# Optimization experiments

Hardware: AMD Instinct MI355X
Metric: run time of the kernel (lower is better)

Reference implementation:

```python
import jax, jax.numpy as jnp
import numpy as np

DIM = 192
HEADS = 6
WIN = 7


def conv2d(x, w, b, pad):
    # x: (N,C,H,W), w: (O,I,kh,kw)
    y = jax.lax.conv_general_dilated(
        x, w, window_strides=(1, 1), padding=[(pad, pad), (pad, pad)],
        dimension_numbers=('NCHW', 'OIHW', 'NCHW'))
    return y + b[None, :, None, None]


def setup_inputs() -> dict:
    key = jax.random.key(0)
    ks = jax.random.split(key, 4)
    B, C, H, W = 8, DIM, 128, 128
    D = C // HEADS
    s = lambda fan_in: 1.0 / np.sqrt(fan_in)
    return {
        'x': jax.random.normal(ks[0], (B, C, H, W), jnp.float32),
        'w_qkv': jax.random.normal(ks[1], (3 * C, C, 1, 1), jnp.float32) * s(C),
        'b_qkv': jnp.zeros((3 * C,), jnp.float32),
        'w_attn': jax.random.normal(ks[2], (WIN * WIN, 2 * D, WIN, WIN), jnp.float32) * s(2 * D * WIN * WIN),
        'b_attn': jnp.zeros((WIN * WIN,), jnp.float32),
        'w_proj': jax.random.normal(ks[3], (C, C, 1, 1), jnp.float32) * s(C),
        'b_proj': jnp.zeros((C,), jnp.float32),
    }


def reference(x, w_qkv, b_qkv, w_attn, b_attn, w_proj, b_proj):
    B, C, H, W = x.shape
    D = C // HEADS
    scale = D ** -0.5
    # qkv 1x1 conv -> (B, 3, heads, D, H, W)
    qkv = conv2d(x, w_qkv, b_qkv, 0).reshape(B, 3, HEADS, D, H, W)
    q, v = qkv[:, 0], qkv[:, 2]  # NOTE: original code uses q twice (not k)
    q_flat = q.reshape(B * HEADS, D, H, W)
    qq = jnp.concatenate([q_flat * scale, q_flat], axis=1)  # (B*heads, 2D, H, W)
    # conv-generated local attention logits over winSize^2 positions
    attn = conv2d(qq, w_attn, b_attn, WIN // 2)
    attn = jax.nn.softmax(attn, axis=1).reshape(B, HEADS, WIN * WIN, H, W)
    # sum over window dim of v (broadcast over k) * attn (broadcast over d)
    out = jnp.einsum('bhkxy,bhdxy->bhdxy', attn, v).reshape(B, C, H, W)
    return conv2d(out, w_proj, b_proj, 0)
```

## Files before the change

### kernel.cpp

```cpp
#include <hip/hip_runtime.h>
#include <stdint.h>
#include <stddef.h>


#define CDIM 192
#define HWPX 16384
#define LDS_STRIDE 200

typedef __attribute__((ext_vector_type(8))) short short8;
typedef __attribute__((ext_vector_type(4))) float floatx4;
typedef __attribute__((ext_vector_type(4))) unsigned short ushort4_t;

__device__ __forceinline__ unsigned short f2bf(float f) {
    union { float f; unsigned int u; } v; v.f = f;
    unsigned int r = (v.u + 0x7FFFu + ((v.u >> 16) & 1u)) >> 16;
    return (unsigned short)r;
}

__global__ __launch_bounds__(192) void prep_kernel(
    const float* __restrict__ w_qkv, const float* __restrict__ b_qkv,
    const float* __restrict__ w_proj, const float* __restrict__ b_proj,
    unsigned short* __restrict__ Mb, float* __restrict__ bias)
{
    const int o = blockIdx.x, c = threadIdx.x;
    const float* wpr = w_proj + o * CDIM;
    const float* wv  = w_qkv + 2 * CDIM * CDIM;
    float acc = 0.f;
    #pragma unroll 32
    for (int k = 0; k < CDIM; ++k)
        acc = fmaf(wpr[k], wv[k * CDIM + c], acc);
    Mb[o * CDIM + c] = f2bf(acc);

    __shared__ float red[CDIM];
    red[c] = wpr[c] * b_qkv[2 * CDIM + c];
    __syncthreads();
    if (c < 64) {
        float v = red[c] + red[c + 64] + red[c + 128];
        #pragma unroll
        for (int off = 32; off > 0; off >>= 1) v += __shfl_down(v, off);
        if (c == 0) bias[o] = v + b_proj[o];
    }
}

__global__ __launch_bounds__(256, 2) void fused_kernel(
    const float* __restrict__ x,
    const unsigned short* __restrict__ Mb,
    const float* __restrict__ bias,
    float* __restrict__ out)
{
    __shared__ unsigned short Xl[64 * LDS_STRIDE];

    const int tid = threadIdx.x;
    const int bid = blockIdx.x;
    const int b   = bid >> 8;
    const int p0  = (bid & 255) << 6;

    const int lane = tid & 63;
    const int w    = tid >> 6;
    const int n    = lane & 15;
    const int q    = lane >> 4;

    const float* xb = x + (size_t)b * CDIM * HWPX + p0;
    #pragma unroll
    for (int it = 0; it < 3; ++it) {
        const int slot = it * 256 + tid;
        const int p4   = slot & 15;
        const int cg4  = slot >> 4;
        const float* src = xb + (size_t)(cg4 * 4) * HWPX + p4 * 4;
        floatx4 f0 = *(const floatx4*)(src);
        floatx4 f1 = *(const floatx4*)(src + HWPX);
        floatx4 f2 = *(const floatx4*)(src + 2 * HWPX);
        floatx4 f3 = *(const floatx4*)(src + 3 * HWPX);
        #pragma unroll
        for (int i = 0; i < 4; ++i) {
            ushort4_t v4;
            v4.x = f2bf(f0[i]); v4.y = f2bf(f1[i]);
            v4.z = f2bf(f2[i]); v4.w = f2bf(f3[i]);
            *(ushort4_t*)&Xl[(p4 * 4 + i) * LDS_STRIDE + cg4 * 4] = v4;
        }
    }
    __syncthreads();

    floatx4 acc[3][4];
    #pragma unroll
    for (int t = 0; t < 3; ++t)
        #pragma unroll
        for (int pt = 0; pt < 4; ++pt)
            acc[t][pt] = (floatx4){0.f, 0.f, 0.f, 0.f};

    #pragma unroll
    for (int t = 0; t < 3; ++t) {
        const int ot = w * 3 + t;
        short8 a[6];
        const unsigned short* arow = Mb + (ot * 16 + n) * CDIM + q * 8;
        #pragma unroll
        for (int ks = 0; ks < 6; ++ks)
            a[ks] = *(const short8*)(arow + ks * 32);
        #pragma unroll
        for (int pt = 0; pt < 4; ++pt) {
            const unsigned short* brow = &Xl[(pt * 16 + n) * LDS_STRIDE + q * 8];
            #pragma unroll
            for (int ks = 0; ks < 6; ++ks) {
                short8 bfr = *(const short8*)(brow + ks * 32);
                acc[t][pt] = __builtin_amdgcn_mfma_f32_16x16x32_bf16(
                    a[ks], bfr, acc[t][pt], 0, 0, 0);
            }
        }
    }

    float* ob = out + (size_t)b * CDIM * HWPX + p0;
    #pragma unroll
    for (int t = 0; t < 3; ++t) {
        const int ot = w * 3 + t;
        #pragma unroll
        for (int r = 0; r < 4; ++r) {
            const int o = ot * 16 + q * 4 + r;
            const float bo = bias[o];
            float* orow = ob + (size_t)o * HWPX + n;
            #pragma unroll
            for (int pt = 0; pt < 4; ++pt)
                orow[pt * 16] = acc[t][pt][r] + bo;
        }
    }
}

extern "C" void kernel_launch(void* const* d_in, const int* in_sizes, int n_in,
                              void* d_out, int out_size, void* d_ws, size_t ws_size,
                              hipStream_t stream) {
    const float* x      = (const float*)d_in[0];
    const float* w_qkv  = (const float*)d_in[1];
    const float* b_qkv  = (const float*)d_in[2];
    const float* w_proj = (const float*)d_in[5];
    const float* b_proj = (const float*)d_in[6];
    float* out = (float*)d_out;

    unsigned short* Mb = (unsigned short*)d_ws;
    float* bias = (float*)((char*)d_ws + CDIM * CDIM * sizeof(unsigned short));

    const int B = in_sizes[0] / (CDIM * HWPX);

    prep_kernel<<<CDIM, CDIM, 0, stream>>>(w_qkv, b_qkv, w_proj, b_proj, Mb, bias);
    fused_kernel<<<B * 256, 256, 0, stream>>>(x, Mb, bias, out);
}
```

Before: 202.4 us.

## Process four pixel tiles per block with double-buffered LDS prefetch

Each block now handles four consecutive 64-pixel tiles. It keeps the weight fragments and bias in registers across tiles, and prefetches the next tile's global data into registers while MFMA and stores run on the current tile, using double-buffered LDS. The goal is to hide global load latency and amortise the weight loads, in a kernel that is memory-bound. The costs are higher register pressure, a quarter as many blocks (512), and possible occupancy loss.

Result: no change. 199.5 us (-1.4%).

```diff
diff --git a/kernel.cpp b/kernel.cpp
--- a/kernel.cpp
+++ b/kernel.cpp
@@ -6,6 +6,7 @@
 #define CDIM 192
 #define HWPX 16384
 #define LDS_STRIDE 200
+#define T_TILES 4
 
 typedef __attribute__((ext_vector_type(8))) short short8;
 typedef __attribute__((ext_vector_type(4))) float floatx4;
@@ -48,79 +49,120 @@
     const float* __restrict__ bias,
     float* __restrict__ out)
 {
-    __shared__ unsigned short Xl[64 * LDS_STRIDE];
+    __shared__ unsigned short Xl[2][64 * LDS_STRIDE];
 
-    const int tid = threadIdx.x;
-    const int bid = blockIdx.x;
-    const int b   = bid >> 8;
-    const int p0  = (bid & 255) << 6;
-
+    const int tid  = threadIdx.x;
     const int lane = tid & 63;
     const int w    = tid >> 6;
     const int n    = lane & 15;
     const int q    = lane >> 4;
 
-    const float* xb = x + (size_t)b * CDIM * HWPX + p0;
-    #pragma unroll
-    for (int it = 0; it < 3; ++it) {
-        const int slot = it * 256 + tid;
-        const int p4   = slot & 15;
-        const int cg4  = slot >> 4;
-        const float* src = xb + (size_t)(cg4 * 4) * HWPX + p4 * 4;
-        floatx4 f0 = *(const floatx4*)(src);
-        floatx4 f1 = *(const floatx4*)(src + HWPX);
-        floatx4 f2 = *(const floatx4*)(src + 2 * HWPX);
-        floatx4 f3 = *(const floatx4*)(src + 3 * HWPX);
+    const int p4  = tid & 15;
+    const int cg0 = tid >> 4;
+
+    const int tile0 = blockIdx.x * T_TILES;
+
+    auto load_tile = [&](int tile, floatx4* fl) {
+        const float* xb = x + (size_t)(tile >> 8) * (CDIM * HWPX)
+                            + ((tile & 255) << 6);
+        const float* src0 = xb + (size_t)(cg0 * 4) * HWPX + p4 * 4;
         #pragma unroll
-        for (int i = 0; i < 4; ++i) {
-            ushort4_t v4;
-            v4.x = f2bf(f0[i]); v4.y = f2bf(f1[i]);
-            v4.z = f2bf(f2[i]); v4.w = f2bf(f3[i]);
-            *(ushort4_t*)&Xl[(p4 * 4 + i) * LDS_STRIDE + cg4 * 4] = v4;
+        for (int it = 0; it < 3; ++it) {
+            const float* src = src0 + (size_t)(it * 64) * HWPX;
+            #pragma unroll
+            for (int j = 0; j < 4; ++j)
+                fl[it * 4 + j] = *(const floatx4*)(src + (size_t)j * HWPX);
         }
-    }
-    __syncthreads();
+    };
 
-    floatx4 acc[3][4];
-    #pragma unroll
-    for (int t = 0; t < 3; ++t)
+    auto stage_tile = [&](int buf, const floatx4* fl) {
         #pragma unroll
-        for (int pt = 0; pt < 4; ++pt)
-            acc[t][pt] = (floatx4){0.f, 0.f, 0.f, 0.f};
+        for (int it = 0; it < 3; ++it) {
+            unsigned short* dst =
+                &Xl[buf][p4 * 4 * LDS_STRIDE + (it * 16 + cg0) * 4];
+            #pragma unroll
+            for (int i = 0; i < 4; ++i) {
+                ushort4_t v4;
+                v4.x = f2bf(fl[it * 4 + 0][i]);
+                v4.y = f2bf(fl[it * 4 + 1][i]);
+                v4.z = f2bf(fl[it * 4 + 2][i]);
+                v4.w = f2bf(fl[it * 4 + 3][i]);
+                *(ushort4_t*)(dst + i * LDS_STRIDE) = v4;
+            }
+        }
+    };
 
+    short8 a[3][6];
+    float  bo[3][4];
     #pragma unroll
     for (int t = 0; t < 3; ++t) {
         const int ot = w * 3 + t;
-        short8 a[6];
         const unsigned short* arow = Mb + (ot * 16 + n) * CDIM + q * 8;
         #pragma unroll
         for (int ks = 0; ks < 6; ++ks)
-            a[ks] = *(const short8*)(arow + ks * 32);
+            a[t][ks] = *(const short8*)(arow + ks * 32);
+        #pragma unroll
+        for (int r = 0; r < 4; ++r)
+            bo[t][r] = bias[ot * 16 + q * 4 + r];
+    }
+
+    floatx4 fl[12];
+
+    load_tile(tile0, fl);
+    stage_tile(0, fl);
+    __syncthreads();
+
+    #pragma unroll
+    for (int t = 0; t < T_TILES; ++t) {
+        const int cur = t & 1;
+
+        if (t + 1 < T_TILES)
+            load_tile(tile0 + t + 1, fl);
+
+        floatx4 acc[3][4];
+        #pragma unroll
+        for (int tt = 0; tt < 3; ++tt)
+            #pragma unroll
+            for (int pt = 0; pt < 4; ++pt)
+                acc[tt][pt] = (floatx4){0.f, 0.f, 0.f, 0.f};
+
         #pragma unroll
         for (int pt = 0; pt < 4; ++pt) {
-            const unsigned short* brow = &Xl[(pt * 16 + n) * LDS_STRIDE + q * 8];
+            const unsigned short* brow =
+                &Xl[cur][(pt * 16 + n) * LDS_STRIDE + q * 8];
+            short8 bfr[6];
             #pragma unroll
-            for (int ks = 0; ks < 6; ++ks) {
-                short8 bfr = *(const short8*)(brow + ks * 32);
-                acc[t][pt] = __builtin_amdgcn_mfma_f32_16x16x32_bf16(
-                    a[ks], bfr, acc[t][pt], 0, 0, 0);
+            for (int ks = 0; ks < 6; ++ks)
+                bfr[ks] = *(const short8*)(brow + ks * 32);
+            #pragma unroll
+            for (int tt = 0; tt < 3; ++tt)
+                #pragma unroll
+                for (int ks = 0; ks < 6; ++ks)
+                    acc[tt][pt] = __builtin_amdgcn_mfma_f32_16x16x32_bf16(
+                        a[tt][ks], bfr[ks], acc[tt][pt], 0, 0, 0);
+        }
+
+        {
+            const int tile = tile0 + t;
+            float* ob = out + (size_t)(tile >> 8) * (CDIM * HWPX)
+                            + ((tile & 255) << 6);
+            #pragma unroll
+            for (int tt = 0; tt < 3; ++tt) {
+                #pragma unroll
+                for (int r = 0; r < 4; ++r) {
+                    const int o = (w * 3 + tt) * 16 + q * 4 + r;
+                    float* orow = ob + (size_t)o * HWPX + n;
+                    #pragma unroll
+                    for (int pt = 0; pt < 4; ++pt)
+                        orow[pt * 16] = acc[tt][pt][r] + bo[tt][r];
+                }
             }
         }
-    }
 
-    float* ob = out + (size_t)b * CDIM * HWPX + p0;
-    #pragma unroll
-    for (int t = 0; t < 3; ++t) {
-        const int ot = w * 3 + t;
-        #pragma unroll
-        for (int r = 0; r < 4; ++r) {
-            const int o = ot * 16 + q * 4 + r;
-            const float bo = bias[o];
-            float* orow = ob + (size_t)o * HWPX + n;
-            #pragma unroll
-            for (int pt = 0; pt < 4; ++pt)
-                orow[pt * 16] = acc[t][pt][r] + bo;
-        }
+        if (t + 1 < T_TILES)
+            stage_tile(cur ^ 1, fl);
+
+        __syncthreads();
     }
 }
 
@@ -140,5 +182,5 @@
     const int B = in_sizes[0] / (CDIM * HWPX);
 
     prep_kernel<<<CDIM, CDIM, 0, stream>>>(w_qkv, b_qkv, w_proj, b_proj, Mb, bias);
-    fused_kernel<<<B * 256, 256, 0, stream>>>(x, Mb, bias, out);
+    fused_kernel<<<(B * 256) / T_TILES, 256, 0, stream>>>(x, Mb, bias, out);
 }
```
